# Kernel optimization log

Measured on AMD Instinct MI355X. Metric: run time of the kernel, lower is better.

## Reference

```python
import jax, jax.numpy as jnp
import numpy as np

B, P, M, CI, CO, W = 8, 16384, 16, 16, 32, 17
RES_RATE = 0.5
SQ_CONV = float(np.sqrt(1.0 - RES_RATE))
SQ_RES = float(np.sqrt(RES_RATE))


def setup_inputs() -> dict:
    key = jax.random.key(0)
    k0, k1, k2, k3, k4 = jax.random.split(key, 5)
    in_pc = jax.random.normal(k0, (B, P, CI), dtype=jnp.float32)
    # neighbor ids in [0, P]; value P is the padding sentinel (masked out)
    neighbor_id = jax.random.randint(k1, (P, M), 0, P + 1)
    weights = jax.random.normal(k2, (W, CO * CI), dtype=jnp.float32)
    bias = jnp.zeros((P, CO), dtype=jnp.float32)  # perpoint_bias == 1
    w_weights = jax.random.normal(k3, (P, M, W), dtype=jnp.float32) / (M * W)
    weight_res = jax.random.normal(k4, (CO, CI), dtype=jnp.float32) / CO
    return {
        "in_pc": in_pc,
        "weights": weights,
        "bias": bias,
        "w_weights": w_weights,
        "weight_res": weight_res,
        "neighbor_id": neighbor_id,
    }


def reference(in_pc, weights, bias, w_weights, weight_res, neighbor_id):
    b = in_pc.shape[0]
    # mask: 1 for real neighbor, 0 for padding sentinel (id == P)
    mask = (neighbor_id != P).astype(in_pc.dtype)  # [P, M]
    # pad point cloud with one zero point so sentinel index gathers zeros
    in_pc_pad = jnp.concatenate(
        [in_pc, jnp.zeros((b, 1, CI), dtype=in_pc.dtype)], axis=1
    )  # [B, P+1, CI]
    in_neighbors = in_pc_pad[:, neighbor_id]  # [B, P, M, CI]
    # per-point conv weights: masked learned combination of basis weights
    ww = w_weights * mask[:, :, None]  # [P, M, W]
    Wpm = jnp.einsum("pmw,wc->pmc", ww, weights).reshape(P, M, CO, CI)
    # gather-generate-matmul: contract neighbors with per-point weights, sum over M
    out_pc_conv = jnp.einsum("pmoi,bpmi->bpo", Wpm, in_neighbors) + bias
    out_pc_conv = jax.nn.elu(out_pc_conv)  # not final layer
    # residual branch: channel projection (in_c != out_c), identity over points
    out_pc_res = jnp.einsum("oi,bpi->bpo", weight_res, in_pc_pad)[:, :P]
    return out_pc_conv * SQ_CONV + out_pc_res * SQ_RES
```

## Files before the change

### kernel.cpp

```cpp
#include <hip/hip_runtime.h>

#define PP 16384
#define SQH 0.70710678118654752440f

typedef unsigned int u32;
typedef unsigned short u16;
typedef __attribute__((ext_vector_type(8))) short bfrag;
typedef __attribute__((ext_vector_type(4))) float ffrag;
typedef __attribute__((ext_vector_type(16))) float ffrag16;
typedef __attribute__((ext_vector_type(4))) float f4;

union BU { bfrag v; uint4 u; };

__device__ __forceinline__ u32 pk2(float a, float b) {
  u32 ua = __float_as_uint(a), ub = __float_as_uint(b);
  return ((ua + 0x8000u) >> 16) | ((ub + 0x8000u) & 0xffff0000u);
}

#define XTB_B ((size_t)(PP + 1) * 256)
#define WB_B  XTB_B
#define WR_B  (XTB_B + 18432)
#define XG_B  (WR_B + 2048)
#define XG_W  (XG_B / 4)

__global__ __launch_bounds__(256) void prep_kernel(
    const float* __restrict__ in_pc, const float* __restrict__ weights,
    const float* __restrict__ weight_res, u32* __restrict__ ws) {
  __shared__ u32 T[64 * 72];
  const int blk = blockIdx.x, t = threadIdx.x;
  if (blk < 256) {
    const int p0 = blk * 64;
    const int pl = t >> 2, i4 = t & 3;
#pragma unroll
    for (int b = 0; b < 8; ++b) {
      f4 v = *(const f4*)(in_pc + ((size_t)b * PP + p0 + pl) * 16 + i4 * 4);
      T[pl * 72 + b * 8 + i4 * 2]     = pk2(v.x, v.y);
      T[pl * 72 + b * 8 + i4 * 2 + 1] = pk2(v.z, v.w);
    }
    __syncthreads();
#pragma unroll
    for (int k = 0; k < 4; ++k) {
      int idx = k * 256 + t;
      int pl2 = idx >> 4, c2 = (idx & 15) * 4;
      uint4 v = *(const uint4*)&T[pl2 * 72 + c2];
      *(uint4*)&ws[(size_t)(p0 + pl2) * 64 + c2] = v;
    }
#pragma unroll
    for (int k = 0; k < 4; ++k) {
      int idx = k * 256 + t;
      int pl2 = idx >> 4, m = idx & 15;
      u32 T0 = T[pl2 * 72 + m];
      u32 T1 = T[pl2 * 72 + 16 + m];
      u32 T2 = T[pl2 * 72 + 32 + m];
      u32 T3 = T[pl2 * 72 + 48 + m];
      uint4 w;
      w.x = (T0 & 0xffffu) | (T1 << 16);
      w.y = (T2 & 0xffffu) | (T3 << 16);
      w.z = (T0 >> 16)     | (T1 & 0xffff0000u);
      w.w = (T2 >> 16)     | (T3 & 0xffff0000u);
      *(uint4*)&ws[XG_W + (size_t)(p0 + pl2) * 64 + m * 4] = w;
    }
    return;
  }
  if (blk == 256 && t < 32) {
    *(uint2*)&ws[(size_t)PP * 64 + t * 2] = make_uint2(0u, 0u);
    *(uint2*)&ws[XG_W + (size_t)PP * 64 + t * 2] = make_uint2(0u, 0u);
  }
  int e = (blk - 256) * 256 + t;
  if (e < 1152) {
    int nt = e / 576, rem = e - nt * 576;
    int ks = rem >> 6, l = rem & 63;
    int quad = l >> 4, n = l & 15;
    int k0 = ks * 32 + quad * 8;
    uint4 pkd = make_uint4(0u, 0u, 0u, 0u);
    if (k0 < 272) {
      int w = k0 >> 4, i0 = k0 & 15;
      const float* src = weights + w * 512 + (nt * 16 + n) * 16 + i0;
      f4 lo = *(const f4*)src;
      f4 hi = *(const f4*)(src + 4);
      pkd = make_uint4(pk2(lo.x, lo.y), pk2(lo.z, lo.w), pk2(hi.x, hi.y), pk2(hi.z, hi.w));
    }
    *(uint4*)((char*)ws + WB_B + (size_t)e * 16) = pkd;
  } else if (e < 1280) {
    int l2 = e - 1152, nt = l2 >> 6, l = l2 & 63;
    int quad = l >> 4, n = l & 15;
    uint4 pkd = make_uint4(0u, 0u, 0u, 0u);
    if (quad < 2) {
      const float* src = weight_res + (nt * 16 + n) * 16 + quad * 8;
      f4 lo = *(const f4*)src;
      f4 hi = *(const f4*)(src + 4);
      pkd = make_uint4(pk2(lo.x, lo.y), pk2(lo.z, lo.w), pk2(hi.x, hi.y), pk2(hi.z, hi.w));
    }
    *(uint4*)((char*)ws + WR_B + (size_t)(e - 1152) * 16) = pkd;
  }
}

__device__ __forceinline__ void gather_pt(u32 (&ad)[4][4], int4 na, int4 nb,
                                          const u16* __restrict__ xG, int col) {
#define GJ(j, r0, r1)                                                        \
  {                                                                          \
    uint2 d = *(const uint2*)(xG + (size_t)(u32)(r0) * 128 + col * 4);       \
    uint2 e = *(const uint2*)(xG + (size_t)(u32)(r1) * 128 + col * 4);       \
    ad[0][j] = (d.x & 0xffffu) | (e.x << 16);                                \
    ad[1][j] = (d.x >> 16)     | (e.x & 0xffff0000u);                        \
    ad[2][j] = (d.y & 0xffffu) | (e.y << 16);                                \
    ad[3][j] = (d.y >> 16)     | (e.y & 0xffff0000u);                        \
  }
  GJ(0, na.x, na.y)
  GJ(1, na.z, na.w)
  GJ(2, nb.x, nb.y)
  GJ(3, nb.z, nb.w)
#undef GJ
}

__global__ __launch_bounds__(256, 4) void pconv_main(
    const u32* __restrict__ ws,
    const float* __restrict__ bias,
    const float* __restrict__ wwg,
    const int*  __restrict__ nidg,
    float* __restrict__ out)
{
  __shared__ __attribute__((aligned(16))) u16 Abuf[4 * 16 * 296];

  const u16*  __restrict__ xTb = (const u16*)ws;
  const u16*  __restrict__ xG  = (const u16*)((const char*)ws + XG_B);
  const uint4* __restrict__ WB = (const uint4*)((const char*)ws + WB_B);
  const uint4* __restrict__ WR = (const uint4*)((const char*)ws + WR_B);

  const int tid = threadIdx.x;
  const int wid = __builtin_amdgcn_readfirstlane(tid >> 6);
  const int lane = tid & 63;
  const int lo16 = lane & 15, quad = lane >> 4;
  const int col = lane & 31, h = lane >> 5;
  u16* __restrict__ Aw = Abuf + wid * (16 * 296);

  const int p0 = (blockIdx.x * 4 + wid) * 2;

  {
    int r = lane >> 2, c = lane & 3;
    *(uint2*)(Aw + r * 296 + 272 + c * 4) = make_uint2(0u, 0u);
  }

  const int* nrow0 = nidg + (size_t)p0 * 16 + h * 8;
  const int* nrow1 = nidg + (size_t)(p0 + 1) * 16 + h * 8;
  int4 n0a = *(const int4*)nrow0;
  int4 n0b = *(const int4*)(nrow0 + 4);
  int4 n1a = *(const int4*)nrow1;
  int4 n1b = *(const int4*)(nrow1 + 4);

  BU bb0, bb1;
  {
    float v0[8], v1[8];
#pragma unroll
    for (int idx = 0; idx < 8; ++idx) {
      float x0 = 0.f, x1 = 0.f;
      if (col < 17) {
        x0 = wwg[(size_t)p0 * 272 + (h * 8 + idx) * 17 + col];
        x1 = wwg[(size_t)(p0 + 1) * 272 + (h * 8 + idx) * 17 + col];
      }
      v0[idx] = x0; v1[idx] = x1;
    }
    bb0.u = make_uint4(pk2(v0[0], v0[1]), pk2(v0[2], v0[3]), pk2(v0[4], v0[5]), pk2(v0[6], v0[7]));
    bb1.u = make_uint4(pk2(v1[0], v1[1]), pk2(v1[2], v1[3]), pk2(v1[4], v1[5]), pk2(v1[6], v1[7]));
  }

  u32 a0[4][4], a1[4][4];
  gather_pt(a0, n0a, n0b, xG, col);
  gather_pt(a1, n1a, n1b, xG, col);

  float blo[4], bhi[4];
#pragma unroll
  for (int j = 0; j < 4; ++j) {
    int p_e = p0 + ((quad * 4 + j) >> 3);
    blo[j] = bias[(size_t)p_e * 32 + lo16];
    bhi[j] = bias[(size_t)p_e * 32 + 16 + lo16];
  }
  BU su;
  su.u = make_uint4(0u, 0u, 0u, 0u);
  {
    const int p_r = p0 + (lo16 >> 3), b_r = lo16 & 7;
    if (quad < 2)
      su.u = *(const uint4*)(xTb + (size_t)p_r * 128 + b_r * 16 + quad * 8);
  }
  BU rb0, rb1;
  rb0.u = WR[lane];
  rb1.u = WR[64 + lane];

#pragma unroll
  for (int pt = 0; pt < 2; ++pt) {
    const u32 (&ad)[4][4] = pt ? a1 : a0;
    BU bb = pt ? bb1 : bb0;
#pragma unroll
    for (int t = 0; t < 4; ++t) {
      BU aa;
      aa.u = make_uint4(ad[t][0], ad[t][1], ad[t][2], ad[t][3]);
      ffrag16 c = {};
      c = __builtin_amdgcn_mfma_f32_32x32x16_bf16(aa.v, bb.v, c, 0, 0, 0);
      if (col < 17) {
#pragma unroll
        for (int q = 0; q < 4; ++q) {
          int r = pt * 8 + 2 * t + (q >> 1);
          int i0 = 4 * h + 8 * (q & 1);
          u16* dst = Aw + r * 296 + col * 16 + i0;
          *(uint2*)dst = make_uint2(pk2(c[4 * q + 0], c[4 * q + 1]),
                                    pk2(c[4 * q + 2], c[4 * q + 3]));
        }
      }
    }
  }

  ffrag acc0 = {0.f, 0.f, 0.f, 0.f}, acc1 = {0.f, 0.f, 0.f, 0.f};
#pragma unroll
  for (int ks = 0; ks < 9; ++ks) {
    bfrag af = *(const bfrag*)(Aw + lo16 * 296 + ks * 32 + quad * 8);
    BU b0, b1;
    b0.u = WB[ks * 64 + lane];
    b1.u = WB[576 + ks * 64 + lane];
    acc0 = __builtin_amdgcn_mfma_f32_16x16x32_bf16(af, b0.v, acc0, 0, 0, 0);
    acc1 = __builtin_amdgcn_mfma_f32_16x16x32_bf16(af, b1.v, acc1, 0, 0, 0);
  }
  ffrag rz = {0.f, 0.f, 0.f, 0.f};
  ffrag res0 = __builtin_amdgcn_mfma_f32_16x16x32_bf16(su.v, rb0.v, rz, 0, 0, 0);
  ffrag res1 = __builtin_amdgcn_mfma_f32_16x16x32_bf16(su.v, rb1.v, rz, 0, 0, 0);

  float* Ef = (float*)Aw;
#pragma unroll
  for (int j = 0; j < 4; ++j) {
    int r = quad * 4 + j;
    float c0 = acc0[j] + blo[j];
    float c1 = acc1[j] + bhi[j];
    float e0 = c0 > 0.f ? c0 : (__expf(c0) - 1.f);
    float e1 = c1 > 0.f ? c1 : (__expf(c1) - 1.f);
    Ef[r * 40 + lo16]      = SQH * e0 + SQH * res0[j];
    Ef[r * 40 + 16 + lo16] = SQH * e1 + SQH * res1[j];
  }
#pragma unroll
  for (int k = 0; k < 2; ++k) {
    int rr = (lane >> 3) + 8 * k;
    int cc = lane & 7;
    f4 v = *(const f4*)(Ef + rr * 40 + cc * 4);
    int p_s = p0 + (rr >> 3), b_s = rr & 7;
    *(f4*)(out + ((size_t)b_s * PP + p_s) * 32 + cc * 4) = v;
  }
}

extern "C" void kernel_launch(void* const* d_in, const int* in_sizes, int n_in,
                              void* d_out, int out_size, void* d_ws, size_t ws_size,
                              hipStream_t stream) {
  const float* in_pc       = (const float*)d_in[0];
  const float* weights     = (const float*)d_in[1];
  const float* bias        = (const float*)d_in[2];
  const float* w_weights   = (const float*)d_in[3];
  const float* weight_res  = (const float*)d_in[4];
  const int*   neighbor_id = (const int*)d_in[5];
  float* out = (float*)d_out;
  u32* ws = (u32*)d_ws;

  hipLaunchKernelGGL(prep_kernel, dim3(261), dim3(256), 0, stream,
                     in_pc, weights, weight_res, ws);
  hipLaunchKernelGGL(pconv_main, dim3(2048), dim3(256), 0, stream,
                     ws, bias, w_weights, neighbor_id, out);
}
```

Before: 103.3 us.

## Process four points per wave and prefetch second pair's gathers during compute

Each wave now handles four points instead of two, halving the grid. All neighbor ids, basis coefficients and residual inputs are loaded up front, and the gathers for the second point pair are issued after the first pair's MFMAs so their latency overlaps the first pair's second-stage GEMM and epilogue. Launch bounds drop from 4 to 3 waves per SIMD to leave room for the extra live registers. The trade is lower occupancy and fewer blocks in exchange for more latency hiding within each wave.

```diff
diff --git a/kernel.cpp b/kernel.cpp
--- a/kernel.cpp
+++ b/kernel.cpp
@@ -113,7 +113,7 @@
 #undef GJ
 }
 
-__global__ __launch_bounds__(256, 4) void pconv_main(
+__global__ __launch_bounds__(256, 3) void pconv_main(
     const u32* __restrict__ ws,
     const float* __restrict__ bias,
     const float* __restrict__ wwg,
@@ -134,113 +134,132 @@
   const int col = lane & 31, h = lane >> 5;
   u16* __restrict__ Aw = Abuf + wid * (16 * 296);
 
-  const int p0 = (blockIdx.x * 4 + wid) * 2;
+  const int pbase = (blockIdx.x * 4 + wid) * 4;
 
   {
     int r = lane >> 2, c = lane & 3;
     *(uint2*)(Aw + r * 296 + 272 + c * 4) = make_uint2(0u, 0u);
   }
 
-  const int* nrow0 = nidg + (size_t)p0 * 16 + h * 8;
-  const int* nrow1 = nidg + (size_t)(p0 + 1) * 16 + h * 8;
-  int4 n0a = *(const int4*)nrow0;
-  int4 n0b = *(const int4*)(nrow0 + 4);
-  int4 n1a = *(const int4*)nrow1;
-  int4 n1b = *(const int4*)(nrow1 + 4);
-
-  BU bb0, bb1;
-  {
-    float v0[8], v1[8];
+  const int* nr = nidg + (size_t)pbase * 16 + h * 8;
+  int4 n0a = *(const int4*)(nr);
+  int4 n0b = *(const int4*)(nr + 4);
+  int4 n1a = *(const int4*)(nr + 16);
+  int4 n1b = *(const int4*)(nr + 20);
+  int4 n2a = *(const int4*)(nr + 32);
+  int4 n2b = *(const int4*)(nr + 36);
+  int4 n3a = *(const int4*)(nr + 48);
+  int4 n3b = *(const int4*)(nr + 52);
+
+  BU bb[4];
+#pragma unroll
+  for (int p = 0; p < 4; ++p) {
+    float v[8];
 #pragma unroll
     for (int idx = 0; idx < 8; ++idx) {
-      float x0 = 0.f, x1 = 0.f;
-      if (col < 17) {
-        x0 = wwg[(size_t)p0 * 272 + (h * 8 + idx) * 17 + col];
-        x1 = wwg[(size_t)(p0 + 1) * 272 + (h * 8 + idx) * 17 + col];
-      }
-      v0[idx] = x0; v1[idx] = x1;
-    }
-    bb0.u = make_uint4(pk2(v0[0], v0[1]), pk2(v0[2], v0[3]), pk2(v0[4], v0[5]), pk2(v0[6], v0[7]));
-    bb1.u = make_uint4(pk2(v1[0], v1[1]), pk2(v1[2], v1[3]), pk2(v1[4], v1[5]), pk2(v1[6], v1[7]));
+      float x = 0.f;
+      if (col < 17)
+        x = wwg[(size_t)(pbase + p) * 272 + (h * 8 + idx) * 17 + col];
+      v[idx] = x;
+    }
+    bb[p].u = make_uint4(pk2(v[0], v[1]), pk2(v[2], v[3]),
+                         pk2(v[4], v[5]), pk2(v[6], v[7]));
+  }
+
+  BU rb0, rb1;
+  rb0.u = WR[lane];
+  rb1.u = WR[64 + lane];
+  BU su[2];
+#pragma unroll
+  for (int pp = 0; pp < 2; ++pp) {
+    su[pp].u = make_uint4(0u, 0u, 0u, 0u);
+    const int p_r = pbase + 2 * pp + (lo16 >> 3), b_r = lo16 & 7;
+    if (quad < 2)
+      su[pp].u = *(const uint4*)(xTb + (size_t)p_r * 128 + b_r * 16 + quad * 8);
   }
 
   u32 a0[4][4], a1[4][4];
   gather_pt(a0, n0a, n0b, xG, col);
   gather_pt(a1, n1a, n1b, xG, col);
 
-  float blo[4], bhi[4];
-#pragma unroll
-  for (int j = 0; j < 4; ++j) {
-    int p_e = p0 + ((quad * 4 + j) >> 3);
-    blo[j] = bias[(size_t)p_e * 32 + lo16];
-    bhi[j] = bias[(size_t)p_e * 32 + 16 + lo16];
-  }
-  BU su;
-  su.u = make_uint4(0u, 0u, 0u, 0u);
-  {
-    const int p_r = p0 + (lo16 >> 3), b_r = lo16 & 7;
-    if (quad < 2)
-      su.u = *(const uint4*)(xTb + (size_t)p_r * 128 + b_r * 16 + quad * 8);
-  }
-  BU rb0, rb1;
-  rb0.u = WR[lane];
-  rb1.u = WR[64 + lane];
-
-#pragma unroll
-  for (int pt = 0; pt < 2; ++pt) {
-    const u32 (&ad)[4][4] = pt ? a1 : a0;
-    BU bb = pt ? bb1 : bb0;
-#pragma unroll
-    for (int t = 0; t < 4; ++t) {
-      BU aa;
-      aa.u = make_uint4(ad[t][0], ad[t][1], ad[t][2], ad[t][3]);
-      ffrag16 c = {};
-      c = __builtin_amdgcn_mfma_f32_32x32x16_bf16(aa.v, bb.v, c, 0, 0, 0);
-      if (col < 17) {
-#pragma unroll
-        for (int q = 0; q < 4; ++q) {
-          int r = pt * 8 + 2 * t + (q >> 1);
-          int i0 = 4 * h + 8 * (q & 1);
-          u16* dst = Aw + r * 296 + col * 16 + i0;
-          *(uint2*)dst = make_uint2(pk2(c[4 * q + 0], c[4 * q + 1]),
-                                    pk2(c[4 * q + 2], c[4 * q + 3]));
+#pragma unroll
+  for (int pp = 0; pp < 2; ++pp) {
+    const int p0 = pbase + 2 * pp;
+
+#pragma unroll
+    for (int pt = 0; pt < 2; ++pt) {
+      const u32 (&ad)[4][4] = pt ? a1 : a0;
+      BU bbv = bb[2 * pp + pt];
+#pragma unroll
+      for (int t = 0; t < 4; ++t) {
+        BU aa;
+        aa.u = make_uint4(ad[t][0], ad[t][1], ad[t][2], ad[t][3]);
+        ffrag16 c = {};
+        c = __builtin_amdgcn_mfma_f32_32x32x16_bf16(aa.v, bbv.v, c, 0, 0, 0);
+        if (col < 17) {
+#pragma unroll
+          for (int q = 0; q < 4; ++q) {
+            int r = pt * 8 + 2 * t + (q >> 1);
+            int i0 = 4 * h + 8 * (q & 1);
+            u16* dst = Aw + r * 296 + col * 16 + i0;
+            *(uint2*)dst = make_uint2(pk2(c[4 * q + 0], c[4 * q + 1]),
+                                      pk2(c[4 * q + 2], c[4 * q + 3]));
+          }
         }
       }
     }
-  }
-
-  ffrag acc0 = {0.f, 0.f, 0.f, 0.f}, acc1 = {0.f, 0.f, 0.f, 0.f};
-#pragma unroll
-  for (int ks = 0; ks < 9; ++ks) {
-    bfrag af = *(const bfrag*)(Aw + lo16 * 296 + ks * 32 + quad * 8);
-    BU b0, b1;
-    b0.u = WB[ks * 64 + lane];
-    b1.u = WB[576 + ks * 64 + lane];
-    acc0 = __builtin_amdgcn_mfma_f32_16x16x32_bf16(af, b0.v, acc0, 0, 0, 0);
-    acc1 = __builtin_amdgcn_mfma_f32_16x16x32_bf16(af, b1.v, acc1, 0, 0, 0);
-  }
-  ffrag rz = {0.f, 0.f, 0.f, 0.f};
-  ffrag res0 = __builtin_amdgcn_mfma_f32_16x16x32_bf16(su.v, rb0.v, rz, 0, 0, 0);
-  ffrag res1 = __builtin_amdgcn_mfma_f32_16x16x32_bf16(su.v, rb1.v, rz, 0, 0, 0);
-
-  float* Ef = (float*)Aw;
-#pragma unroll
-  for (int j = 0; j < 4; ++j) {
-    int r = quad * 4 + j;
-    float c0 = acc0[j] + blo[j];
-    float c1 = acc1[j] + bhi[j];
-    float e0 = c0 > 0.f ? c0 : (__expf(c0) - 1.f);
-    float e1 = c1 > 0.f ? c1 : (__expf(c1) - 1.f);
-    Ef[r * 40 + lo16]      = SQH * e0 + SQH * res0[j];
-    Ef[r * 40 + 16 + lo16] = SQH * e1 + SQH * res1[j];
-  }
-#pragma unroll
-  for (int k = 0; k < 2; ++k) {
-    int rr = (lane >> 3) + 8 * k;
-    int cc = lane & 7;
-    f4 v = *(const f4*)(Ef + rr * 40 + cc * 4);
-    int p_s = p0 + (rr >> 3), b_s = rr & 7;
-    *(f4*)(out + ((size_t)b_s * PP + p_s) * 32 + cc * 4) = v;
+
+    if (pp == 0) {
+      gather_pt(a0, n2a, n2b, xG, col);
+      gather_pt(a1, n3a, n3b, xG, col);
+    }
+
+    float blo[4], bhi[4];
+#pragma unroll
+    for (int j = 0; j < 4; ++j) {
+      int p_e = p0 + ((quad * 4 + j) >> 3);
+      blo[j] = bias[(size_t)p_e * 32 + lo16];
+      bhi[j] = bias[(size_t)p_e * 32 + 16 + lo16];
+    }
+
+    ffrag acc0 = {0.f, 0.f, 0.f, 0.f}, acc1 = {0.f, 0.f, 0.f, 0.f};
+#pragma unroll
+    for (int ks = 0; ks < 9; ++ks) {
+      bfrag af = *(const bfrag*)(Aw + lo16 * 296 + ks * 32 + quad * 8);
+      BU b0, b1;
+      b0.u = WB[ks * 64 + lane];
+      b1.u = WB[576 + ks * 64 + lane];
+      acc0 = __builtin_amdgcn_mfma_f32_16x16x32_bf16(af, b0.v, acc0, 0, 0, 0);
+      acc1 = __builtin_amdgcn_mfma_f32_16x16x32_bf16(af, b1.v, acc1, 0, 0, 0);
+    }
+    ffrag rz = {0.f, 0.f, 0.f, 0.f};
+    ffrag res0 = __builtin_amdgcn_mfma_f32_16x16x32_bf16(su[pp].v, rb0.v, rz, 0, 0, 0);
+    ffrag res1 = __builtin_amdgcn_mfma_f32_16x16x32_bf16(su[pp].v, rb1.v, rz, 0, 0, 0);
+
+    float* Ef = (float*)Aw;
+#pragma unroll
+    for (int j = 0; j < 4; ++j) {
+      int r = quad * 4 + j;
+      float c0 = acc0[j] + blo[j];
+      float c1 = acc1[j] + bhi[j];
+      float e0 = c0 > 0.f ? c0 : (__expf(c0) - 1.f);
+      float e1 = c1 > 0.f ? c1 : (__expf(c1) - 1.f);
+      Ef[r * 40 + lo16]      = SQH * e0 + SQH * res0[j];
+      Ef[r * 40 + 16 + lo16] = SQH * e1 + SQH * res1[j];
+    }
+#pragma unroll
+    for (int k = 0; k < 2; ++k) {
+      int rr = (lane >> 3) + 8 * k;
+      int cc = lane & 7;
+      f4 v = *(const f4*)(Ef + rr * 40 + cc * 4);
+      int p_s = p0 + (rr >> 3), b_s = rr & 7;
+      *(f4*)(out + ((size_t)b_s * PP + p_s) * 32 + cc * 4) = v;
+    }
+
+    if (pp == 0) {
+      int r = lane >> 2, c = lane & 3;
+      *(uint2*)(Aw + r * 296 + 272 + c * 4) = make_uint2(0u, 0u);
+    }
   }
 }
 
@@ -258,6 +277,6 @@
 
   hipLaunchKernelGGL(prep_kernel, dim3(261), dim3(256), 0, stream,
                      in_pc, weights, weight_res, ws);
-  hipLaunchKernelGGL(pconv_main, dim3(2048), dim3(256), 0, stream,
+  hipLaunchKernelGGL(pconv_main, dim3(1024), dim3(256), 0, stream,
                      ws, bias, w_weights, neighbor_id, out);
 }
```

Result: slower. 107.9 us (+4.4%).
